# Optimization experiments

Hardware: AMD Instinct MI355X
Metric: run time of the kernel (lower is better)

Reference implementation:

```python
import jax, jax.numpy as jnp
import numpy as np
from jax import lax

PART = 224   # PART_IMAGE_SIZE
PAD = 224    # PAD_SIZE
TOPN = 4
IOU_THRESH = 0.25
N_ANCHORS = 1614


def _conv(x, w, b, stride, pad):
    y = lax.conv_general_dilated(x, w, (stride, stride), [(pad, pad), (pad, pad)],
                                 dimension_numbers=('NCHW', 'OIHW', 'NCHW'))
    return y + b[None, :, None, None]


def _iou(box, boxes):
    # box [4], boxes [N,4] as (y0,x0,y1,x1)
    yy0 = jnp.maximum(box[0], boxes[:, 0]); xx0 = jnp.maximum(box[1], boxes[:, 1])
    yy1 = jnp.minimum(box[2], boxes[:, 2]); xx1 = jnp.minimum(box[3], boxes[:, 3])
    inter = jnp.clip(yy1 - yy0, 0.0) * jnp.clip(xx1 - xx0, 0.0)
    a = (box[2] - box[0]) * (box[3] - box[1])
    areas = (boxes[:, 2] - boxes[:, 0]) * (boxes[:, 3] - boxes[:, 1])
    return inter / (a + areas - inter)


def _nms(scores, boxes):
    # hard NMS keeping TOPN boxes; returns indices [TOPN]
    valid = jnp.ones(scores.shape, dtype=bool)
    idxs = []
    for _ in range(TOPN):
        i = jnp.argmax(jnp.where(valid, scores, -jnp.inf))
        idxs.append(i)
        valid = valid & (_iou(boxes[i], boxes) <= IOU_THRESH)
    return jnp.stack(idxs)


def _crop_resize(img, box):
    # img [3,Hp,Wp] padded image, box [4] float; bilinear, align_corners=True,
    # matching F.interpolate(x_pad[:, :, y0:y1, x0:x1], (PART, PART))
    Hp, Wp = img.shape[1], img.shape[2]
    def coords(c0, c1, L):
        t = jnp.arange(PART, dtype=img.dtype) / (PART - 1)
        c = c0 + (c1 - 1.0 - c0) * t          # absolute source coordinate
        cf = jnp.floor(c)
        lo = jnp.clip(cf.astype(jnp.int32), 0, L - 1)
        hi = jnp.clip(lo + 1, 0, L - 1)
        return lo, hi, c - cf
    yl, yh, wy = coords(box[0], box[2], Hp)
    xl, xh, wx = coords(box[1], box[3], Wp)
    g = lambda yi, xi: img[:, yi[:, None], xi[None, :]]   # [3,PART,PART]
    return ((1 - wy)[:, None] * ((1 - wx) * g(yl, xl) + wx * g(yl, xh))
            + wy[:, None] * ((1 - wx) * g(yh, xl) + wx * g(yh, xh)))


def setup_inputs() -> dict:
    key = jax.random.key(0)
    ks = jax.random.split(key, 20)
    x = jax.random.uniform(ks[0], (16, 3, 448, 448), dtype=jnp.float32)
    rpn_feature = jax.random.normal(ks[1], (16, 2048, 14, 14), dtype=jnp.float32)
    # valid boxes inside the padded 896x896 image
    y0 = jax.random.randint(ks[2], (N_ANCHORS,), 0, 560)
    x0 = jax.random.randint(ks[3], (N_ANCHORS,), 0, 560)
    h = jax.random.randint(ks[4], (N_ANCHORS,), 32, 336)
    w = jax.random.randint(ks[5], (N_ANCHORS,), 32, 336)
    anchors = jnp.stack([y0, x0, jnp.minimum(y0 + h, 896), jnp.minimum(x0 + w, 896)], axis=1).astype(jnp.int32)
    s = 0.02
    inp = {
        'x': x, 'rpn_feature': rpn_feature, 'anchors': anchors,
        'w_down1': jax.random.normal(ks[6], (128, 2048, 3, 3), jnp.float32) * s,
        'b_down1': jnp.zeros((128,), jnp.float32),
        'w_down2': jax.random.normal(ks[7], (128, 128, 3, 3), jnp.float32) * s,
        'b_down2': jnp.zeros((128,), jnp.float32),
        'w_down3': jax.random.normal(ks[8], (128, 128, 3, 3), jnp.float32) * s,
        'b_down3': jnp.zeros((128,), jnp.float32),
        'w_tidy1': jax.random.normal(ks[9], (6, 128, 1, 1), jnp.float32) * s,
        'b_tidy1': jnp.zeros((6,), jnp.float32),
        'w_tidy2': jax.random.normal(ks[10], (6, 128, 1, 1), jnp.float32) * s,
        'b_tidy2': jnp.zeros((6,), jnp.float32),
        'w_tidy3': jax.random.normal(ks[11], (9, 128, 1, 1), jnp.float32) * s,
        'b_tidy3': jnp.zeros((9,), jnp.float32),
    }
    return inp


def reference(x, rpn_feature, anchors,
              w_down1, b_down1, w_down2, b_down2, w_down3, b_down3,
              w_tidy1, b_tidy1, w_tidy2, b_tidy2, w_tidy3, b_tidy3):
    B = x.shape[0]
    # ProposalNet
    d1 = jax.nn.relu(_conv(rpn_feature, w_down1, b_down1, 1, 1))   # [B,128,14,14]
    d2 = jax.nn.relu(_conv(d1, w_down2, b_down2, 2, 1))            # [B,128,7,7]
    d3 = jax.nn.relu(_conv(d2, w_down3, b_down3, 2, 1))            # [B,128,4,4]
    t1 = _conv(d1, w_tidy1, b_tidy1, 1, 0).reshape(B, -1)
    t2 = _conv(d2, w_tidy2, b_tidy2, 1, 0).reshape(B, -1)
    t3 = _conv(d3, w_tidy3, b_tidy3, 1, 0).reshape(B, -1)
    rpn_score = jnp.concatenate([t1, t2, t3], axis=1)              # [B, 1614]
    boxes = anchors.astype(x.dtype)                                # [N,4]
    top_n_index = jax.vmap(lambda s: _nms(s, boxes))(rpn_score)    # [B,TOPN]
    top_n_prob = jnp.take_along_axis(rpn_score, top_n_index, axis=1)
    x_pad = jnp.pad(x, ((0, 0), (0, 0), (PAD, PAD), (PAD, PAD)))   # [B,3,896,896]
    sel_boxes = boxes[top_n_index]                                 # [B,TOPN,4]
    part_imgs = jax.vmap(lambda img, bxs: jax.vmap(lambda b: _crop_resize(img, b))(bxs))(x_pad, sel_boxes)
    # part_imgs: [B,TOPN,3,PART,PART]
    return rpn_score, top_n_index, top_n_prob, part_imgs
```

## Files before the change

kernel.cpp:

```cpp
#include <hip/hip_runtime.h>
#include <hip/hip_bf16.h>

#define NB 16
#define NA 1614

typedef __bf16 bf16x8 __attribute__((ext_vector_type(8)));
typedef float f32x4 __attribute__((ext_vector_type(4)));

__device__ __forceinline__ unsigned short f2bf(float v) {
  unsigned u = __float_as_uint(v);
  unsigned r = (u + 0x7FFFu + ((u >> 16) & 1u)) >> 16;
  return (unsigned short)r;
}
__device__ __forceinline__ float bf2f(unsigned short s) {
  return __uint_as_float(((unsigned)s) << 16);
}

__global__ void prep_w(const float* __restrict__ w, unsigned short* __restrict__ wTh,
                       unsigned short* __restrict__ wTl) {
  int e = blockIdx.x * 256 + threadIdx.x;
  if (e >= 9 * 128 * 2048) return;
  int tap = e / (128 * 2048);
  int rem = e - tap * (128 * 2048);
  int oc = rem >> 11, ic = rem & 2047;
  float v = w[((size_t)oc * 2048 + ic) * 9 + tap];
  unsigned short h = f2bf(v);
  wTh[e] = h;
  wTl[e] = f2bf(v - bf2f(h));
}

__global__ __launch_bounds__(256)
void prep_a(const float* __restrict__ in, unsigned short* __restrict__ aTh,
            unsigned short* __restrict__ aTl) {
  const int bid = blockIdx.x;
  const int chunk = bid & 63, b = bid >> 6;
  __shared__ float s[32 * 200];
  const float* src = in + ((size_t)b * 2048 + chunk * 32) * 196;
#pragma unroll
  for (int r = 0; r < 7; r++) {
    int e = threadIdx.x + 256 * r;
    if (e < 1568) {
      int ic = e / 49, f = e - ic * 49;
      float4 v = ((const float4*)(src + (size_t)ic * 196))[f];
      *(float4*)(s + ic * 200 + f * 4) = v;
    }
  }
  __syncthreads();
  unsigned short* oh = aTh + (size_t)bid * 196 * 32;
  unsigned short* ol = aTl + (size_t)bid * 196 * 32;
#pragma unroll
  for (int r = 0; r < 4; r++) {
    int e = threadIdx.x + 256 * r;
    if (e < 784) {
      int g = e / 196, pos = e - g * 196;
      unsigned short hv[8], lv[8];
#pragma unroll
      for (int j = 0; j < 8; j++) {
        float v = s[(g * 8 + j) * 200 + pos];
        unsigned short h = f2bf(v);
        hv[j] = h;
        lv[j] = f2bf(v - bf2f(h));
      }
      *(uint4*)(oh + (size_t)pos * 32 + g * 8) = *(uint4*)hv;
      *(uint4*)(ol + (size_t)pos * 32 + g * 8) = *(uint4*)lv;
    }
  }
}

__global__ __launch_bounds__(256, 3)
void conv1_mfma(const unsigned short* __restrict__ aTh, const unsigned short* __restrict__ aTl,
                const unsigned short* __restrict__ wTh, const unsigned short* __restrict__ wTl,
                float* __restrict__ p1) {
  const int bid = blockIdx.x;
  const int b  = bid & 15;
  const int nh = (bid >> 4) & 1;
  const int kc = bid >> 5;
  const int tid = threadIdx.x;
  const int wid = tid >> 6, lane = tid & 63;
  const int wm = wid & 1, wn = wid >> 1;
  const int q = lane >> 4, ln = lane & 15;

  __shared__ unsigned short sAh[256 * 40];
  __shared__ unsigned short sAl[256 * 40];
  __shared__ unsigned short sBh[64 * 40];
  __shared__ unsigned short sBl[64 * 40];

  for (int e = tid; e < 5120; e += 256) {
    ((unsigned int*)sAh)[e] = 0u;
    ((unsigned int*)sAl)[e] = 0u;
  }

  int abase[7];
#pragma unroll
  for (int mf = 0; mf < 7; mf++) {
    int row = wm * 112 + mf * 16 + ln;
    int y = row / 14, x = row - y * 14;
    abase[mf] = ((row < 196) ? (y * 16 + x) : 0) * 40 + q * 8;
  }

  f32x4 acc[7][2];
#pragma unroll
  for (int mf = 0; mf < 7; mf++)
#pragma unroll
    for (int nf = 0; nf < 2; nf++) acc[mf][nf] = (f32x4){0.f, 0.f, 0.f, 0.f};

  const int boc = tid >> 2, bic0 = (tid & 3) * 8;
  const size_t bocbase = (size_t)(nh * 64 + boc) << 11;

  uint4 pvh, pvl;
  {
    size_t g = bocbase + kc * 128 + bic0;
    pvh = *(const uint4*)(wTh + g);
    pvl = *(const uint4*)(wTl + g);
  }

  for (int it = 0; it < 36; it++) {
    const int ks = it / 9, tap = it - ks * 9;
    __syncthreads();
    *(uint4*)(sBh + boc * 40 + bic0) = pvh;
    *(uint4*)(sBl + boc * 40 + bic0) = pvl;
    if (tap == 0) {
      const uint4* gh = (const uint4*)(aTh + ((size_t)(b * 64 + kc * 4 + ks) * 196) * 32);
      const uint4* gl = (const uint4*)(aTl + ((size_t)(b * 64 + kc * 4 + ks) * 196) * 32);
#pragma unroll
      for (int r = 0; r < 4; r++) {
        int e = tid + 256 * r;
        if (e < 784) {
          int slot = e >> 2, part = e & 3;
          int py = slot / 14, px = slot - py * 14;
          int dst = ((py + 1) * 16 + px + 1) * 40 + part * 8;
          *(uint4*)(sAh + dst) = gh[e];
          *(uint4*)(sAl + dst) = gl[e];
        }
      }
    }
    {
      const int nit = (it < 35) ? it + 1 : 35;
      const int ks2 = nit / 9, tap2 = nit - ks2 * 9;
      size_t g = (size_t)tap2 * (128 * 2048) + bocbase + kc * 128 + ks2 * 32 + bic0;
      pvh = *(const uint4*)(wTh + g);
      pvl = *(const uint4*)(wTl + g);
    }
    __syncthreads();

    const int t40 = ((tap / 3) * 16 + (tap % 3)) * 40;
    bf16x8 bh[2], bl[2];
#pragma unroll
    for (int nf = 0; nf < 2; nf++) {
      const int bb = (wn * 32 + nf * 16 + ln) * 40 + q * 8;
      bh[nf] = *(const bf16x8*)(sBh + bb);
      bl[nf] = *(const bf16x8*)(sBl + bb);
    }
#pragma unroll
    for (int mf = 0; mf < 7; mf++) {
      bf16x8 ah = *(const bf16x8*)(sAh + abase[mf] + t40);
      bf16x8 al = *(const bf16x8*)(sAl + abase[mf] + t40);
#pragma unroll
      for (int nf = 0; nf < 2; nf++) {
        acc[mf][nf] = __builtin_amdgcn_mfma_f32_16x16x32_bf16(ah, bh[nf], acc[mf][nf], 0, 0, 0);
        acc[mf][nf] = __builtin_amdgcn_mfma_f32_16x16x32_bf16(al, bh[nf], acc[mf][nf], 0, 0, 0);
        acc[mf][nf] = __builtin_amdgcn_mfma_f32_16x16x32_bf16(ah, bl[nf], acc[mf][nf], 0, 0, 0);
      }
    }
  }

  float* pk = p1 + ((size_t)kc * NB + b) * 196 * 128;
#pragma unroll
  for (int mf = 0; mf < 7; mf++) {
    const int row0 = wm * 112 + mf * 16 + q * 4;
#pragma unroll
    for (int nf = 0; nf < 2; nf++) {
      const int oc = nh * 64 + wn * 32 + nf * 16 + ln;
#pragma unroll
      for (int r = 0; r < 4; r++) {
        const int row = row0 + r;
        if (row < 196) pk[(size_t)row * 128 + oc] = acc[mf][nf][r];
      }
    }
  }
}

__global__ void conv1_finish_p(const float* __restrict__ p1, const float* __restrict__ bias,
                               float* __restrict__ d1) {
  const int i = blockIdx.x * 256 + threadIdx.x;
  if (i >= NB * 196 * 128) return;
  const int oc = i & 127;
  const int t = i >> 7;
  const int pos = t % 196, b = t / 196;
  float s = bias[oc];
#pragma unroll
  for (int k = 0; k < 16; k++) s += p1[(size_t)k * (NB * 196 * 128) + i];
  d1[((size_t)b * 128 + oc) * 196 + pos] = fmaxf(s, 0.f);
}

__global__ void conv2_part(const float* __restrict__ d1, const float* __restrict__ w,
                           float* __restrict__ p2) {
  const int bid = blockIdx.x;
  const int kc = bid & 3, oct = (bid >> 2) & 3, b = bid >> 4;
  const int ic0 = kc * 32, oc0 = oct * 32;
  const int tid = threadIdx.x;
  const int ocl = tid >> 3, rw = tid & 7;

  __shared__ float s_in[32 * 320];
  __shared__ float s_w[32 * 324];

#pragma unroll
  for (int r = 0; r < 32; r++) {
    const int e = tid + 256 * r;
    const int ch = e >> 8, idx = e & 255;
    const int tr = idx >> 4, tc = idx & 15;
    const int iy = tr - 1, ix = tc - 1;
    float v = 0.f;
    if ((unsigned)iy < 14u && (unsigned)ix < 14u)
      v = d1[((size_t)b * 128 + ic0 + ch) * 196 + iy * 14 + ix];
    s_in[ch * 320 + tr * 20 + tc] = v;
  }
#pragma unroll
  for (int r = 0; r < 36; r++) {
    const int e = tid + 256 * r;
    const int oc = e / 288, rem = e - oc * 288;
    const int ch = rem / 9, tap = rem - ch * 9;
    s_w[ch * 324 + tap * 36 + oc] =
        w[(size_t)(oc0 + oc) * 1152 + (size_t)ic0 * 9 + rem];
  }
  __syncthreads();

  if (rw < 7) {
    float acc[7] = {};
    for (int ic = 0; ic < 32; ic++) {
      const float* wrow = s_w + ic * 324 + ocl;
      const float* irow = s_in + ic * 320;
#pragma unroll
      for (int ky = 0; ky < 3; ky++) {
        const float* r = irow + (2 * rw + ky) * 20;
        const float4 f0 = *(const float4*)(r);
        const float4 f1 = *(const float4*)(r + 4);
        const float4 f2 = *(const float4*)(r + 8);
        const float4 f3 = *(const float4*)(r + 12);
        const float ev[8] = {f0.x, f0.z, f1.x, f1.z, f2.x, f2.z, f3.x, f3.z};
        const float od[7] = {f0.y, f0.w, f1.y, f1.w, f2.y, f2.w, f3.y};
        const float w0 = wrow[(ky * 3 + 0) * 36];
        const float w1 = wrow[(ky * 3 + 1) * 36];
        const float w2 = wrow[(ky * 3 + 2) * 36];
#pragma unroll
        for (int x = 0; x < 7; x++)
          acc[x] = fmaf(w0, ev[x], fmaf(w1, od[x], fmaf(w2, ev[x + 1], acc[x])));
      }
    }
    float* po = p2 + (((size_t)kc * NB + b) * 128 + oc0 + ocl) * 49 + rw * 7;
#pragma unroll
    for (int x = 0; x < 7; x++) po[x] = acc[x];
  }
}

__global__ void conv2_finish(const float* __restrict__ p2, const float* __restrict__ bias,
                             float* __restrict__ d2) {
  const int i = blockIdx.x * 256 + threadIdx.x;
  if (i >= NB * 128 * 49) return;
  const int oc = (i / 49) & 127;
  float s = bias[oc];
#pragma unroll
  for (int k = 0; k < 4; k++) s += p2[(size_t)k * (NB * 128 * 49) + i];
  d2[i] = fmaxf(s, 0.f);
}

__global__ void conv3_part(const float* __restrict__ d2, const float* __restrict__ w,
                           float* __restrict__ p3) {
  const int bid = blockIdx.x;
  const int kc = bid & 1, oct = (bid >> 1) & 7, b = bid >> 4;
  const int ic0 = kc * 64, oc0 = oct * 16;
  const int tid = threadIdx.x;
  const int oc = tid >> 4, p = tid & 15;
  const int y = p >> 2, x = p & 3;

  __shared__ float s_in[64 * 108];
  __shared__ float s_w[64 * 144];

#pragma unroll
  for (int r = 0; r < 21; r++) {
    const int e = tid + 256 * r;
    if (e < 64 * 81) {
      const int ch = e / 81, idx = e - ch * 81;
      const int tr = idx / 9, tc = idx - tr * 9;
      const int iy = tr - 1, ix = tc - 1;
      float v = 0.f;
      if ((unsigned)iy < 7u && (unsigned)ix < 7u)
        v = d2[((size_t)b * 128 + ic0 + ch) * 49 + iy * 7 + ix];
      s_in[ch * 108 + tr * 12 + tc] = v;
    }
  }
#pragma unroll
  for (int r = 0; r < 36; r++) {
    const int e = tid + 256 * r;
    const int o = e / 576, rem = e - o * 576;
    const int ch = rem / 9, tap = rem - ch * 9;
    s_w[ch * 144 + tap * 16 + o] =
        w[(size_t)(oc0 + o) * 1152 + (size_t)ic0 * 9 + rem];
  }
  __syncthreads();

  float acc = 0.f;
  for (int ic = 0; ic < 64; ic++) {
    const float* wrow = s_w + ic * 144 + oc;
    const float* irow = s_in + ic * 108 + 2 * y * 12 + 2 * x;
#pragma unroll
    for (int ky = 0; ky < 3; ky++)
#pragma unroll
      for (int kx = 0; kx < 3; kx++)
        acc = fmaf(wrow[(ky * 3 + kx) * 16], irow[ky * 12 + kx], acc);
  }
  p3[(((size_t)kc * NB + b) * 128 + oc0 + oc) * 16 + p] = acc;
}

__global__ void conv3_finish(const float* __restrict__ p3, const float* __restrict__ bias,
                             float* __restrict__ d3) {
  const int i = blockIdx.x * 256 + threadIdx.x;
  if (i >= NB * 128 * 16) return;
  const int oc = (i >> 4) & 127;
  float s = bias[oc] + p3[i] + p3[(size_t)(NB * 128 * 16) + i];
  d3[i] = fmaxf(s, 0.f);
}

__global__ __launch_bounds__(256, 1)
void score_nms(const float* __restrict__ d1, const float* __restrict__ d2,
               const float* __restrict__ d3,
               const float* __restrict__ w1, const float* __restrict__ b1,
               const float* __restrict__ w2, const float* __restrict__ b2,
               const float* __restrict__ w3, const float* __restrict__ b3,
               const int* __restrict__ anchors, float* __restrict__ score,
               float* __restrict__ out_idx, float* __restrict__ out_prob,
               float* __restrict__ sel) {
  __shared__ float s_in[32 * 200];
  __shared__ float s_w[21 * 128];
  __shared__ float s_b[21];
  __shared__ float s_sc[NA];
  __shared__ float s_bx[NA * 4];
  __shared__ float r_s[256];
  __shared__ int r_i[256];
  const int b = blockIdx.x, tid = threadIdx.x;

  for (int i = tid; i < 768; i += 256) s_w[i] = w1[i];
  for (int i = tid; i < 768; i += 256) s_w[768 + i] = w2[i];
  for (int i = tid; i < 1152; i += 256) s_w[1536 + i] = w3[i];
  if (tid < 21) s_b[tid] = (tid < 6) ? b1[tid] : (tid < 12) ? b2[tid - 6] : b3[tid - 12];
  for (int i = tid; i < NA; i += 256) {
    s_bx[i * 4 + 0] = (float)anchors[i * 4 + 0];
    s_bx[i * 4 + 1] = (float)anchors[i * 4 + 1];
    s_bx[i * 4 + 2] = (float)anchors[i * 4 + 2];
    s_bx[i * 4 + 3] = (float)anchors[i * 4 + 3];
  }

  float acc[5] = {0.f, 0.f, 0.f, 0.f, 0.f};
  for (int chunk = 0; chunk < 4; chunk++) {
    __syncthreads();
    const float* src = d1 + ((size_t)b * 128 + chunk * 32) * 196;
#pragma unroll
    for (int r = 0; r < 7; r++) {
      int e = tid + 256 * r;
      if (e < 1568) {
        int ic = e / 49, f = e - ic * 49;
        *(float4*)(s_in + ic * 200 + f * 4) = ((const float4*)(src + (size_t)ic * 196))[f];
      }
    }
    __syncthreads();
#pragma unroll
    for (int k = 0; k < 5; k++) {
      int j = tid + 256 * k;
      if (j < 1176) {
        int oc = j / 196, p = j - oc * 196;
        const float* wr = s_w + oc * 128 + chunk * 32;
        float s = acc[k];
#pragma unroll
        for (int ic = 0; ic < 32; ic++) s = fmaf(wr[ic], s_in[ic * 200 + p], s);
        acc[k] = s;
      }
    }
  }
#pragma unroll
  for (int k = 0; k < 5; k++) {
    int j = tid + 256 * k;
    if (j < 1176) {
      int oc = j / 196;
      float s = acc[k] + s_b[oc];
      s_sc[j] = s;
      score[b * NA + j] = s;
    }
  }

  __syncthreads();
  {
    const float* src = d2 + (size_t)b * 6272;
#pragma unroll
    for (int r = 0; r < 7; r++) {
      int e = tid + 256 * r;
      if (e < 1568) *(float4*)(s_in + e * 4) = ((const float4*)src)[e];
    }
  }
  __syncthreads();
#pragma unroll
  for (int k = 0; k < 2; k++) {
    int jj = tid + 256 * k;
    if (jj < 294) {
      int oc = jj / 49, p = jj - oc * 49;
      const float* wr = s_w + 768 + oc * 128;
      float s = s_b[6 + oc];
#pragma unroll 8
      for (int ic = 0; ic < 128; ic++) s = fmaf(wr[ic], s_in[ic * 49 + p], s);
      s_sc[1176 + jj] = s;
      score[b * NA + 1176 + jj] = s;
    }
  }

  __syncthreads();
  {
    const float* src = d3 + (size_t)b * 2048;
#pragma unroll
    for (int r = 0; r < 2; r++) {
      int e = tid + 256 * r;
      if (e < 512) *(float4*)(s_in + e * 4) = ((const float4*)src)[e];
    }
  }
  __syncthreads();
  if (tid < 144) {
    int oc = tid >> 4, p = tid & 15;
    const float* wr = s_w + 1536 + oc * 128;
    float s = s_b[12 + oc];
#pragma unroll 8
    for (int ic = 0; ic < 128; ic++) s = fmaf(wr[ic], s_in[ic * 16 + p], s);
    s_sc[1470 + tid] = s;
    score[b * NA + 1470 + tid] = s;
  }
  __syncthreads();

  for (int t = 0; t < 4; t++) {
    float bs = -__builtin_inff();
    int bi = NA;
    for (int i = tid; i < NA; i += 256) {
      float s = s_sc[i];
      if (s > bs || (s == bs && i < bi)) { bs = s; bi = i; }
    }
    r_s[tid] = bs; r_i[tid] = bi;
    __syncthreads();
    for (int off = 128; off > 0; off >>= 1) {
      if (tid < off) {
        float s2 = r_s[tid + off]; int i2 = r_i[tid + off];
        if (s2 > r_s[tid] || (s2 == r_s[tid] && i2 < r_i[tid])) { r_s[tid] = s2; r_i[tid] = i2; }
      }
      __syncthreads();
    }
    const int idx = r_i[0];
    const float by0 = s_bx[idx * 4 + 0], bx0 = s_bx[idx * 4 + 1];
    const float by1 = s_bx[idx * 4 + 2], bx1 = s_bx[idx * 4 + 3];
    if (tid == 0) {
      out_idx[b * 4 + t] = (float)idx;
      out_prob[b * 4 + t] = s_sc[idx];
      sel[(b * 4 + t) * 4 + 0] = by0;
      sel[(b * 4 + t) * 4 + 1] = bx0;
      sel[(b * 4 + t) * 4 + 2] = by1;
      sel[(b * 4 + t) * 4 + 3] = bx1;
    }
    __syncthreads();
    const float a = (by1 - by0) * (bx1 - bx0);
    for (int i = tid; i < NA; i += 256) {
      float cy0 = s_bx[i * 4 + 0], cx0 = s_bx[i * 4 + 1];
      float cy1 = s_bx[i * 4 + 2], cx1 = s_bx[i * 4 + 3];
      float yy0 = fmaxf(by0, cy0), xx0 = fmaxf(bx0, cx0);
      float yy1 = fminf(by1, cy1), xx1 = fminf(bx1, cx1);
      float inter = fmaxf(yy1 - yy0, 0.f) * fmaxf(xx1 - xx0, 0.f);
      float ar = (cy1 - cy0) * (cx1 - cx0);
      float iou = inter / (a + ar - inter);
      if (iou > 0.25f) s_sc[i] = -__builtin_inff();
    }
    __syncthreads();
  }
}

__global__ void crop_kernel(const float* __restrict__ x, const float* __restrict__ sel,
                            float* __restrict__ out) {
  long long i = (long long)blockIdx.x * 256 + threadIdx.x;
  const long long total = (long long)NB * 4 * 3 * 224 * 224;
  if (i >= total) return;
  int px = (int)(i % 224);
  long long t = i / 224;
  int py = (int)(t % 224); t /= 224;
  int ch = (int)(t % 3);  t /= 3;
  int n  = (int)(t % 4);
  int b  = (int)(t / 4);

  const float* bx = sel + (b * 4 + n) * 4;
  const float y0 = bx[0], x0 = bx[1], y1 = bx[2], x1 = bx[3];

  float ty = (float)py / 223.0f;
  float cy = y0 + (y1 - 1.0f - y0) * ty;
  float cyf = floorf(cy);
  int ylo = (int)cyf; ylo = ylo < 0 ? 0 : (ylo > 895 ? 895 : ylo);
  int yhi = ylo + 1 > 895 ? 895 : ylo + 1;
  float wy = cy - cyf;

  float tx = (float)px / 223.0f;
  float cx = x0 + (x1 - 1.0f - x0) * tx;
  float cxf = floorf(cx);
  int xlo = (int)cxf; xlo = xlo < 0 ? 0 : (xlo > 895 ? 895 : xlo);
  int xhi = xlo + 1 > 895 ? 895 : xlo + 1;
  float wx = cx - cxf;

  const float* img = x + ((size_t)b * 3 + ch) * 448 * 448;
  auto g = [&](int yy, int xx) -> float {
    yy -= 224; xx -= 224;
    if ((unsigned)yy < 448u && (unsigned)xx < 448u)
      return img[(size_t)yy * 448 + xx];
    return 0.f;
  };
  float v00 = g(ylo, xlo), v01 = g(ylo, xhi);
  float v10 = g(yhi, xlo), v11 = g(yhi, xhi);
  float r = (1.f - wy) * ((1.f - wx) * v00 + wx * v01) +
            wy * ((1.f - wx) * v10 + wx * v11);
  out[i] = r;
}

extern "C" void kernel_launch(void* const* d_in, const int* in_sizes, int n_in,
                              void* d_out, int out_size, void* d_ws, size_t ws_size,
                              hipStream_t stream) {
  const float* x    = (const float*)d_in[0];
  const float* rpn  = (const float*)d_in[1];
  const int*   anc  = (const int*)d_in[2];
  const float* w_d1 = (const float*)d_in[3];
  const float* b_d1 = (const float*)d_in[4];
  const float* w_d2 = (const float*)d_in[5];
  const float* b_d2 = (const float*)d_in[6];
  const float* w_d3 = (const float*)d_in[7];
  const float* b_d3 = (const float*)d_in[8];
  const float* w_t1 = (const float*)d_in[9];
  const float* b_t1 = (const float*)d_in[10];
  const float* w_t2 = (const float*)d_in[11];
  const float* b_t2 = (const float*)d_in[12];
  const float* w_t3 = (const float*)d_in[13];
  const float* b_t3 = (const float*)d_in[14];

  float* out = (float*)d_out;
  float* ws = (float*)d_ws;

  float* d1  = ws;
  float* d2  = d1 + 401408;
  float* d3  = d2 + 100352;
  float* sel = d3 + 32768;
  float* p2  = sel + 256;
  float* p3  = p2 + 401408;
  unsigned short* wTh = (unsigned short*)(p3 + 65536);
  unsigned short* wTl = wTh + 2359296;
  unsigned short* aTh = wTl + 2359296;
  unsigned short* aTl = aTh + 6422528;

  float* score    = out;
  float* out_idx  = out + 25824;
  float* out_prob = out + 25888;
  float* parts    = out + 25952;
  float* p1       = parts;

  prep_w<<<dim3(9216), dim3(256), 0, stream>>>(w_d1, wTh, wTl);
  prep_a<<<dim3(1024), dim3(256), 0, stream>>>(rpn, aTh, aTl);
  conv1_mfma<<<dim3(512), dim3(256), 0, stream>>>(aTh, aTl, wTh, wTl, p1);
  conv1_finish_p<<<dim3(1568), dim3(256), 0, stream>>>(p1, b_d1, d1);
  conv2_part<<<dim3(256), dim3(256), 0, stream>>>(d1, w_d2, p2);
  conv2_finish<<<dim3(392), dim3(256), 0, stream>>>(p2, b_d2, d2);
  conv3_part<<<dim3(256), dim3(256), 0, stream>>>(d2, w_d3, p3);
  conv3_finish<<<dim3(128), dim3(256), 0, stream>>>(p3, b_d3, d3);
  score_nms<<<dim3(16), dim3(256), 0, stream>>>(d1, d2, d3, w_t1, b_t1, w_t2, b_t2,
                                                w_t3, b_t3, anc, score, out_idx, out_prob, sel);
  crop_kernel<<<dim3(37632), dim3(256), 0, stream>>>(x, sel, parts);
}
```

Baseline: 299.6 us.

## Fuse prep kernels, relayout conv1 LDS tiles, vectorize finish and crop kernels

Merges the weight and activation bf16 split kernels into one launch and rewrites the activation transpose with a padded LDS stride. The conv1 MFMA shared-memory tiles move from a padded row layout to a k-quarter-major layout so fragment loads hit LDS with fewer bank conflicts. The conv1 reduction kernel now uses float4 loads and an LDS transpose for coalesced NCHW writes. The conv3 finish is folded into score_nms, and crop_kernel writes four output pixels per thread with float4 stores. Together these cut launch count and aim to improve memory coalescing, at the cost of fewer blocks in the finish kernel.

Measured after the change: 282.2 us. -5.8%, faster.

```diff
diff --git a/kernel.cpp b/kernel.cpp
--- a/kernel.cpp
+++ b/kernel.cpp
@@ -3,6 +3,7 @@
 
 #define NB 16
 #define NA 1614
+#define NBP (NB * 196 * 128)
 
 typedef __bf16 bf16x8 __attribute__((ext_vector_type(8)));
 typedef float f32x4 __attribute__((ext_vector_type(4)));
@@ -16,53 +17,55 @@
   return __uint_as_float(((unsigned)s) << 16);
 }
 
-__global__ void prep_w(const float* __restrict__ w, unsigned short* __restrict__ wTh,
-                       unsigned short* __restrict__ wTl) {
-  int e = blockIdx.x * 256 + threadIdx.x;
-  if (e >= 9 * 128 * 2048) return;
-  int tap = e / (128 * 2048);
-  int rem = e - tap * (128 * 2048);
-  int oc = rem >> 11, ic = rem & 2047;
-  float v = w[((size_t)oc * 2048 + ic) * 9 + tap];
-  unsigned short h = f2bf(v);
-  wTh[e] = h;
-  wTl[e] = f2bf(v - bf2f(h));
-}
-
 __global__ __launch_bounds__(256)
-void prep_a(const float* __restrict__ in, unsigned short* __restrict__ aTh,
-            unsigned short* __restrict__ aTl) {
+void prep(const float* __restrict__ w, const float* __restrict__ in,
+          unsigned short* __restrict__ wTh, unsigned short* __restrict__ wTl,
+          unsigned short* __restrict__ aTh, unsigned short* __restrict__ aTl) {
+  __shared__ float s[32 * 201];
   const int bid = blockIdx.x;
-  const int chunk = bid & 63, b = bid >> 6;
-  __shared__ float s[32 * 200];
-  const float* src = in + ((size_t)b * 2048 + chunk * 32) * 196;
-#pragma unroll
-  for (int r = 0; r < 7; r++) {
-    int e = threadIdx.x + 256 * r;
-    if (e < 1568) {
-      int ic = e / 49, f = e - ic * 49;
-      float4 v = ((const float4*)(src + (size_t)ic * 196))[f];
-      *(float4*)(s + ic * 200 + f * 4) = v;
-    }
-  }
-  __syncthreads();
-  unsigned short* oh = aTh + (size_t)bid * 196 * 32;
-  unsigned short* ol = aTl + (size_t)bid * 196 * 32;
-#pragma unroll
-  for (int r = 0; r < 4; r++) {
-    int e = threadIdx.x + 256 * r;
-    if (e < 784) {
-      int g = e / 196, pos = e - g * 196;
-      unsigned short hv[8], lv[8];
-#pragma unroll
-      for (int j = 0; j < 8; j++) {
-        float v = s[(g * 8 + j) * 200 + pos];
-        unsigned short h = f2bf(v);
-        hv[j] = h;
-        lv[j] = f2bf(v - bf2f(h));
-      }
-      *(uint4*)(oh + (size_t)pos * 32 + g * 8) = *(uint4*)hv;
-      *(uint4*)(ol + (size_t)pos * 32 + g * 8) = *(uint4*)lv;
+  if (bid < 1024) {
+    const int chunk = bid & 63, b = bid >> 6;
+    const float* src = in + ((size_t)b * 2048 + chunk * 32) * 196;
+#pragma unroll
+    for (int r = 0; r < 7; r++) {
+      int e = threadIdx.x + 256 * r;
+      if (e < 1568) {
+        int ic = e / 49, f = e - ic * 49;
+        float4 v = ((const float4*)(src + (size_t)ic * 196))[f];
+        float* d = s + ic * 201 + f * 4;
+        d[0] = v.x; d[1] = v.y; d[2] = v.z; d[3] = v.w;
+      }
+    }
+    __syncthreads();
+    unsigned short* oh = aTh + (size_t)bid * (196 * 32);
+    unsigned short* ol = aTl + (size_t)bid * (196 * 32);
+#pragma unroll
+    for (int r = 0; r < 4; r++) {
+      int e = threadIdx.x + 256 * r;
+      if (e < 784) {
+        int pos = e >> 2, part = e & 3;
+        unsigned short hv[8], lv[8];
+#pragma unroll
+        for (int j = 0; j < 8; j++) {
+          float v = s[(part * 8 + j) * 201 + pos];
+          unsigned short h = f2bf(v);
+          hv[j] = h;
+          lv[j] = f2bf(v - bf2f(h));
+        }
+        ((uint4*)oh)[e] = *(uint4*)hv;
+        ((uint4*)ol)[e] = *(uint4*)lv;
+      }
+    }
+  } else {
+    int e = (bid - 1024) * 256 + threadIdx.x;
+    if (e < 9 * 128 * 2048) {
+      int tap = e / (128 * 2048);
+      int rem = e - tap * (128 * 2048);
+      int oc = rem >> 11, ic = rem & 2047;
+      float v = w[((size_t)oc * 2048 + ic) * 9 + tap];
+      unsigned short h = f2bf(v);
+      wTh[e] = h;
+      wTl[e] = f2bf(v - bf2f(h));
     }
   }
 }
@@ -80,12 +83,12 @@
   const int wm = wid & 1, wn = wid >> 1;
   const int q = lane >> 4, ln = lane & 15;
 
-  __shared__ unsigned short sAh[256 * 40];
-  __shared__ unsigned short sAl[256 * 40];
-  __shared__ unsigned short sBh[64 * 40];
-  __shared__ unsigned short sBl[64 * 40];
-
-  for (int e = tid; e < 5120; e += 256) {
+  __shared__ unsigned short sAh[4 * 2048];
+  __shared__ unsigned short sAl[4 * 2048];
+  __shared__ unsigned short sBh[4 * 512];
+  __shared__ unsigned short sBl[4 * 512];
+
+  for (int e = tid; e < 4096; e += 256) {
     ((unsigned int*)sAh)[e] = 0u;
     ((unsigned int*)sAl)[e] = 0u;
   }
@@ -95,8 +98,9 @@
   for (int mf = 0; mf < 7; mf++) {
     int row = wm * 112 + mf * 16 + ln;
     int y = row / 14, x = row - y * 14;
-    abase[mf] = ((row < 196) ? (y * 16 + x) : 0) * 40 + q * 8;
-  }
+    abase[mf] = ((row < 196) ? (y * 16 + x) : 0) * 8;
+  }
+  const int qoff = q * 2048;
 
   f32x4 acc[7][2];
 #pragma unroll
@@ -104,12 +108,12 @@
 #pragma unroll
     for (int nf = 0; nf < 2; nf++) acc[mf][nf] = (f32x4){0.f, 0.f, 0.f, 0.f};
 
-  const int boc = tid >> 2, bic0 = (tid & 3) * 8;
+  const int boc = tid >> 2, bicq = tid & 3;
   const size_t bocbase = (size_t)(nh * 64 + boc) << 11;
 
   uint4 pvh, pvl;
   {
-    size_t g = bocbase + kc * 128 + bic0;
+    size_t g = bocbase + kc * 128 + bicq * 8;
     pvh = *(const uint4*)(wTh + g);
     pvl = *(const uint4*)(wTl + g);
   }
@@ -117,8 +121,8 @@
   for (int it = 0; it < 36; it++) {
     const int ks = it / 9, tap = it - ks * 9;
     __syncthreads();
-    *(uint4*)(sBh + boc * 40 + bic0) = pvh;
-    *(uint4*)(sBl + boc * 40 + bic0) = pvl;
+    *(uint4*)(sBh + bicq * 512 + boc * 8) = pvh;
+    *(uint4*)(sBl + bicq * 512 + boc * 8) = pvl;
     if (tap == 0) {
       const uint4* gh = (const uint4*)(aTh + ((size_t)(b * 64 + kc * 4 + ks) * 196) * 32);
       const uint4* gl = (const uint4*)(aTl + ((size_t)(b * 64 + kc * 4 + ks) * 196) * 32);
@@ -126,9 +130,9 @@
       for (int r = 0; r < 4; r++) {
         int e = tid + 256 * r;
         if (e < 784) {
-          int slot = e >> 2, part = e & 3;
-          int py = slot / 14, px = slot - py * 14;
-          int dst = ((py + 1) * 16 + px + 1) * 40 + part * 8;
+          int pos = e >> 2, part = e & 3;
+          int py = pos / 14, px = pos - py * 14;
+          int dst = part * 2048 + ((py + 1) * 16 + px + 1) * 8;
           *(uint4*)(sAh + dst) = gh[e];
           *(uint4*)(sAl + dst) = gl[e];
         }
@@ -137,24 +141,24 @@
     {
       const int nit = (it < 35) ? it + 1 : 35;
       const int ks2 = nit / 9, tap2 = nit - ks2 * 9;
-      size_t g = (size_t)tap2 * (128 * 2048) + bocbase + kc * 128 + ks2 * 32 + bic0;
+      size_t g = (size_t)tap2 * (128 * 2048) + bocbase + kc * 128 + ks2 * 32 + bicq * 8;
       pvh = *(const uint4*)(wTh + g);
       pvl = *(const uint4*)(wTl + g);
     }
     __syncthreads();
 
-    const int t40 = ((tap / 3) * 16 + (tap % 3)) * 40;
+    const int t8 = ((tap / 3) * 16 + (tap % 3)) * 8;
     bf16x8 bh[2], bl[2];
 #pragma unroll
     for (int nf = 0; nf < 2; nf++) {
-      const int bb = (wn * 32 + nf * 16 + ln) * 40 + q * 8;
+      const int bb = q * 512 + (wn * 32 + nf * 16 + ln) * 8;
       bh[nf] = *(const bf16x8*)(sBh + bb);
       bl[nf] = *(const bf16x8*)(sBl + bb);
     }
 #pragma unroll
     for (int mf = 0; mf < 7; mf++) {
-      bf16x8 ah = *(const bf16x8*)(sAh + abase[mf] + t40);
-      bf16x8 al = *(const bf16x8*)(sAl + abase[mf] + t40);
+      bf16x8 ah = *(const bf16x8*)(sAh + qoff + abase[mf] + t8);
+      bf16x8 al = *(const bf16x8*)(sAl + qoff + abase[mf] + t8);
 #pragma unroll
       for (int nf = 0; nf < 2; nf++) {
         acc[mf][nf] = __builtin_amdgcn_mfma_f32_16x16x32_bf16(ah, bh[nf], acc[mf][nf], 0, 0, 0);
@@ -180,17 +184,44 @@
   }
 }
 
-__global__ void conv1_finish_p(const float* __restrict__ p1, const float* __restrict__ bias,
-                               float* __restrict__ d1) {
-  const int i = blockIdx.x * 256 + threadIdx.x;
-  if (i >= NB * 196 * 128) return;
-  const int oc = i & 127;
-  const int t = i >> 7;
-  const int pos = t % 196, b = t / 196;
-  float s = bias[oc];
-#pragma unroll
-  for (int k = 0; k < 16; k++) s += p1[(size_t)k * (NB * 196 * 128) + i];
-  d1[((size_t)b * 128 + oc) * 196 + pos] = fmaxf(s, 0.f);
+__global__ __launch_bounds__(256)
+void conv1_finish_p(const float* __restrict__ p1, const float* __restrict__ bias,
+                    float* __restrict__ d1) {
+  __shared__ float s[28 * 132];
+  const int bid = blockIdx.x;
+  const int pt = bid % 7, b = bid / 7;
+  const int tid = threadIdx.x;
+#pragma unroll
+  for (int r = 0; r < 4; r++) {
+    int u = tid + 256 * r;
+    if (u < 896) {
+      int pos = u >> 5, oc4 = u & 31;
+      const float* base = p1 + ((size_t)(b * 196 + pt * 28 + pos)) * 128 + oc4 * 4;
+      float4 sum = ((const float4*)bias)[oc4];
+#pragma unroll
+      for (int k = 0; k < 16; k++) {
+        float4 v = *(const float4*)(base + (size_t)k * NBP);
+        sum.x += v.x; sum.y += v.y; sum.z += v.z; sum.w += v.w;
+      }
+      sum.x = fmaxf(sum.x, 0.f); sum.y = fmaxf(sum.y, 0.f);
+      sum.z = fmaxf(sum.z, 0.f); sum.w = fmaxf(sum.w, 0.f);
+      *(float4*)(s + pos * 132 + oc4 * 4) = sum;
+    }
+  }
+  __syncthreads();
+#pragma unroll
+  for (int r = 0; r < 4; r++) {
+    int u = tid + 256 * r;
+    if (u < 896) {
+      int oc = u / 7, f = u - oc * 7;
+      float4 v;
+      v.x = s[(f * 4 + 0) * 132 + oc];
+      v.y = s[(f * 4 + 1) * 132 + oc];
+      v.z = s[(f * 4 + 2) * 132 + oc];
+      v.w = s[(f * 4 + 3) * 132 + oc];
+      *(float4*)(d1 + ((size_t)b * 128 + oc) * 196 + pt * 28 + f * 4) = v;
+    }
+  }
 }
 
 __global__ void conv2_part(const float* __restrict__ d1, const float* __restrict__ w,
@@ -312,18 +343,9 @@
   p3[(((size_t)kc * NB + b) * 128 + oc0 + oc) * 16 + p] = acc;
 }
 
-__global__ void conv3_finish(const float* __restrict__ p3, const float* __restrict__ bias,
-                             float* __restrict__ d3) {
-  const int i = blockIdx.x * 256 + threadIdx.x;
-  if (i >= NB * 128 * 16) return;
-  const int oc = (i >> 4) & 127;
-  float s = bias[oc] + p3[i] + p3[(size_t)(NB * 128 * 16) + i];
-  d3[i] = fmaxf(s, 0.f);
-}
-
 __global__ __launch_bounds__(256, 1)
 void score_nms(const float* __restrict__ d1, const float* __restrict__ d2,
-               const float* __restrict__ d3,
+               const float* __restrict__ p3, const float* __restrict__ bd3,
                const float* __restrict__ w1, const float* __restrict__ b1,
                const float* __restrict__ w2, const float* __restrict__ b2,
                const float* __restrict__ w3, const float* __restrict__ b3,
@@ -413,11 +435,21 @@
 
   __syncthreads();
   {
-    const float* src = d3 + (size_t)b * 2048;
+    const float4* s0 = (const float4*)(p3 + (size_t)b * 2048);
+    const float4* s1 = (const float4*)(p3 + 32768 + (size_t)b * 2048);
 #pragma unroll
     for (int r = 0; r < 2; r++) {
       int e = tid + 256 * r;
-      if (e < 512) *(float4*)(s_in + e * 4) = ((const float4*)src)[e];
+      if (e < 512) {
+        float4 a = s0[e], c = s1[e];
+        float bb = bd3[e >> 2];
+        float4 v;
+        v.x = fmaxf(a.x + c.x + bb, 0.f);
+        v.y = fmaxf(a.y + c.y + bb, 0.f);
+        v.z = fmaxf(a.z + c.z + bb, 0.f);
+        v.w = fmaxf(a.w + c.w + bb, 0.f);
+        *(float4*)(s_in + e * 4) = v;
+      }
     }
   }
   __syncthreads();
@@ -477,15 +509,15 @@
 
 __global__ void crop_kernel(const float* __restrict__ x, const float* __restrict__ sel,
                             float* __restrict__ out) {
-  long long i = (long long)blockIdx.x * 256 + threadIdx.x;
-  const long long total = (long long)NB * 4 * 3 * 224 * 224;
-  if (i >= total) return;
-  int px = (int)(i % 224);
-  long long t = i / 224;
-  int py = (int)(t % 224); t /= 224;
-  int ch = (int)(t % 3);  t /= 3;
-  int n  = (int)(t % 4);
-  int b  = (int)(t / 4);
+  int i4 = blockIdx.x * 256 + threadIdx.x;
+  const int total4 = NB * 4 * 3 * 224 * 56;
+  if (i4 >= total4) return;
+  int px0 = (i4 % 56) * 4;
+  int t = i4 / 56;
+  int py = t % 224; t /= 224;
+  int ch = t % 3;  t /= 3;
+  int n  = t % 4;
+  int b  = t / 4;
 
   const float* bx = sel + (b * 4 + n) * 4;
   const float y0 = bx[0], x0 = bx[1], y1 = bx[2], x1 = bx[3];
@@ -496,13 +528,6 @@
   int ylo = (int)cyf; ylo = ylo < 0 ? 0 : (ylo > 895 ? 895 : ylo);
   int yhi = ylo + 1 > 895 ? 895 : ylo + 1;
   float wy = cy - cyf;
-
-  float tx = (float)px / 223.0f;
-  float cx = x0 + (x1 - 1.0f - x0) * tx;
-  float cxf = floorf(cx);
-  int xlo = (int)cxf; xlo = xlo < 0 ? 0 : (xlo > 895 ? 895 : xlo);
-  int xhi = xlo + 1 > 895 ? 895 : xlo + 1;
-  float wx = cx - cxf;
 
   const float* img = x + ((size_t)b * 3 + ch) * 448 * 448;
   auto g = [&](int yy, int xx) -> float {
@@ -511,11 +536,23 @@
       return img[(size_t)yy * 448 + xx];
     return 0.f;
   };
-  float v00 = g(ylo, xlo), v01 = g(ylo, xhi);
-  float v10 = g(yhi, xlo), v11 = g(yhi, xhi);
-  float r = (1.f - wy) * ((1.f - wx) * v00 + wx * v01) +
+
+  float4 res;
+  float* rp = &res.x;
+#pragma unroll
+  for (int k = 0; k < 4; k++) {
+    float tx = (float)(px0 + k) / 223.0f;
+    float cx = x0 + (x1 - 1.0f - x0) * tx;
+    float cxf = floorf(cx);
+    int xlo = (int)cxf; xlo = xlo < 0 ? 0 : (xlo > 895 ? 895 : xlo);
+    int xhi = xlo + 1 > 895 ? 895 : xlo + 1;
+    float wx = cx - cxf;
+    float v00 = g(ylo, xlo), v01 = g(ylo, xhi);
+    float v10 = g(yhi, xlo), v11 = g(yhi, xhi);
+    rp[k] = (1.f - wy) * ((1.f - wx) * v00 + wx * v01) +
             wy * ((1.f - wx) * v10 + wx * v11);
-  out[i] = r;
+  }
+  *(float4*)(out + (size_t)i4 * 4) = res;
 }
 
 extern "C" void kernel_launch(void* const* d_in, const int* in_sizes, int n_in,
@@ -557,15 +594,13 @@
   float* parts    = out + 25952;
   float* p1       = parts;
 
-  prep_w<<<dim3(9216), dim3(256), 0, stream>>>(w_d1, wTh, wTl);
-  prep_a<<<dim3(1024), dim3(256), 0, stream>>>(rpn, aTh, aTl);
+  prep<<<dim3(10240), dim3(256), 0, stream>>>(w_d1, rpn, wTh, wTl, aTh, aTl);
   conv1_mfma<<<dim3(512), dim3(256), 0, stream>>>(aTh, aTl, wTh, wTl, p1);
-  conv1_finish_p<<<dim3(1568), dim3(256), 0, stream>>>(p1, b_d1, d1);
+  conv1_finish_p<<<dim3(112), dim3(256), 0, stream>>>(p1, b_d1, d1);
   conv2_part<<<dim3(256), dim3(256), 0, stream>>>(d1, w_d2, p2);
   conv2_finish<<<dim3(392), dim3(256), 0, stream>>>(p2, b_d2, d2);
   conv3_part<<<dim3(256), dim3(256), 0, stream>>>(d2, w_d3, p3);
-  conv3_finish<<<dim3(128), dim3(256), 0, stream>>>(p3, b_d3, d3);
-  score_nms<<<dim3(16), dim3(256), 0, stream>>>(d1, d2, d3, w_t1, b_t1, w_t2, b_t2,
+  score_nms<<<dim3(16), dim3(256), 0, stream>>>(d1, d2, p3, b_d3, w_t1, b_t1, w_t2, b_t2,
                                                 w_t3, b_t3, anc, score, out_idx, out_prob, sel);
-  crop_kernel<<<dim3(37632), dim3(256), 0, stream>>>(x, sel, parts);
-}
+  crop_kernel<<<dim3(9408), dim3(256), 0, stream>>>(x, sel, parts);
+}
```
